# Kernel optimization log

Hardware: AMD Instinct MI355X
Metric: run time of the kernel (lower is better)

## Reference

```python
import jax, jax.numpy as jnp
import numpy as np
from jax import lax

DN = ('NCHW', 'OIHW', 'NCHW')


def convbn(x, w, s, b, relu=True):
    # conv (no bias) + folded BatchNorm affine (+ optional ReLU)
    y = lax.conv_general_dilated(x, w, (1, 1), 'SAME', dimension_numbers=DN)
    y = y * s[None, :, None, None] + b[None, :, None, None]
    return jnp.maximum(y, 0.0) if relu else y


_PARAM_SHAPES = [
    ('t', (128, 256, 3, 3)), ('l', (128, 256, 3, 3)),
    ('b', (128, 256, 3, 3)), ('r', (128, 256, 3, 3)),
    ('tl3', (256, 128, 3, 3)), ('br3', (256, 128, 3, 3)),
    ('tl1', (256, 256, 1, 1)), ('br1', (256, 256, 1, 1)),
    ('tlo', (256, 256, 3, 3)), ('bro', (256, 256, 3, 3)),
]


def setup_inputs() -> dict:
    key = jax.random.key(0)
    B, C, H, W = 8, 256, 128, 128
    ks = jax.random.split(key, 3 * len(_PARAM_SHAPES) + 1)
    inp = {'x': jax.random.normal(ks[0], (B, C, H, W), jnp.float32)}
    i = 1
    for name, shape in _PARAM_SHAPES:
        cout = shape[0]
        inp['w_' + name] = jax.random.normal(ks[i], shape, jnp.float32) * 0.05
        inp['s_' + name] = 1.0 + 0.1 * jax.random.normal(ks[i + 1], (cout,), jnp.float32)
        inp['b_' + name] = 0.1 * jax.random.normal(ks[i + 2], (cout,), jnp.float32)
        i += 3
    return inp


def reference(x, w_t, s_t, b_t, w_l, s_l, b_l, w_b, s_b, b_b, w_r, s_r, b_r,
              w_tl3, s_tl3, b_tl3, w_br3, s_br3, b_br3,
              w_tl1, s_tl1, b_tl1, w_br1, s_br1, b_br1,
              w_tlo, s_tlo, b_tlo, w_bro, s_bro, b_bro):
    # directional corner pools = (reverse-)cummax along H (axis 2) or W (axis 3)
    t = convbn(x, w_t, s_t, b_t)
    tp = lax.cummax(t, axis=2, reverse=True)   # top_pool: max over rows >= h
    l = convbn(x, w_l, s_l, b_l)
    lp = lax.cummax(l, axis=3, reverse=True)   # left_pool: max over cols >= w
    bo = convbn(x, w_b, s_b, b_b)
    bp = lax.cummax(bo, axis=2)                # bottom_pool: max over rows <= h
    r = convbn(x, w_r, s_r, b_r)
    rp = lax.cummax(r, axis=3)                 # right_pool: max over cols <= w

    tl = convbn(tp + lp, w_tl3, s_tl3, b_tl3, relu=False)
    tl = jnp.maximum(tl + convbn(x, w_tl1, s_tl1, b_tl1, relu=False), 0.0)
    out_tl = convbn(tl, w_tlo, s_tlo, b_tlo)

    br = convbn(bp + rp, w_br3, s_br3, b_br3, relu=False)
    br = jnp.maximum(br + convbn(x, w_br1, s_br1, b_br1, relu=False), 0.0)
    out_br = convbn(br, w_bro, s_bro, b_bro)
    return out_tl, out_br
```

## Files before the change

### kernel.cpp

```cpp
#include <hip/hip_runtime.h>
#include <cstdint>
#include <cstddef>


typedef float  f32x4 __attribute__((ext_vector_type(4)));
typedef float  f4v   __attribute__((ext_vector_type(4)));
typedef short  s16x8 __attribute__((ext_vector_type(8)));
typedef unsigned short u16x4 __attribute__((ext_vector_type(4)));

__device__ __forceinline__ float bf2f(unsigned short u) {
    unsigned x = ((unsigned)u) << 16;
    return __builtin_bit_cast(float, x);
}
__device__ __forceinline__ unsigned short f2bf(float f) {
    unsigned u = __builtin_bit_cast(unsigned, f);
    unsigned r = (u + 0x7fffu + ((u >> 16) & 1u)) >> 16;
    return (unsigned short)r;
}

#define GL_LDS(gp, lp) __builtin_amdgcn_global_load_lds( \
    (const __attribute__((address_space(1))) unsigned int*)(const void*)(gp), \
    (__attribute__((address_space(3))) unsigned int*)(void*)(lp), 16, 0, 0)

template<int CIN, int COUT, bool RELU, bool OUTF32, bool SWZ>
__global__ __launch_bounds__(256, 4)
void conv3_mfma(const unsigned short* __restrict__ in,
                const unsigned short* __restrict__ wpk,
                const float* __restrict__ sc, const float* __restrict__ bi,
                void* __restrict__ outv)
{
    __shared__ unsigned short lds[2][8704];
    const int tid  = threadIdx.x;
    const int lane = tid & 63;
    const int wv   = tid >> 6;
    const int c    = lane & 15;
    const int g    = lane >> 4;

    constexpr int GX  = (COUT / 128) * 2;
    int gx, hy, n;
    if (SWZ) {
        constexpr int NWG = GX * 64 * 8;
        constexpr int Q   = NWG / 8;
        const int braw = blockIdx.x + GX * (blockIdx.y + 64 * blockIdx.z);
        const int wl   = (braw & 7) * Q + (braw >> 3);
        gx = wl % GX;
        const int rest = wl / GX;
        hy = rest & 63;
        n  = rest >> 6;
    } else {
        gx = blockIdx.x; hy = blockIdx.y; n = blockIdx.z;
    }
    const int wtile  = gx & 1;
    const int octile = gx >> 1;
    const int h0   = hy * 2;
    const int w0   = wtile * 64;
    const int r    = wv >> 1;
    const int ocbase = octile * 128 + (wv & 1) * 64;
    const int ocf0   = octile * 8 + (wv & 1) * 4;

    int addrB[3];
    #pragma unroll
    for (int kx = 0; kx < 3; ++kx) {
        int ps0 = c + kx;
        addrB[kx] = r * 4224 + ps0 * 64 + ((g ^ ((ps0 >> 1) & 3)) << 4);
    }

    int so[5];
    #pragma unroll
    for (int it = 0; it < 5; ++it) {
        int u   = it * 256 + tid;
        int row = u / 264;
        int rem = u - row * 264;
        int ps  = rem >> 2;
        int s   = rem & 3;
        int icq = s ^ ((ps >> 1) & 3);
        so[it] = ((n * 130 + h0 + row) * 130 + (w0 + ps)) * CIN + icq * 8;
    }

    auto STAGE = [&](int chunk, int bsel) {
        const unsigned short* bp = in + chunk * 32;
        char* lb = (char*)lds + bsel * 17408 + tid * 16;
        #pragma unroll
        for (int it = 0; it < 4; ++it)
            GL_LDS(bp + so[it], lb + it * 4096);
        if (wv == 0)
            GL_LDS(bp + so[4], lb + 16384);
    };

    f32x4 acc[4][4];
    #pragma unroll
    for (int m = 0; m < 4; ++m)
        #pragma unroll
        for (int p = 0; p < 4; ++p) acc[m][p] = 0.0f;

    const int NC = CIN / 32;
    STAGE(0, 0);
    __syncthreads();

    for (int chunk = 0; chunk < NC; ++chunk) {
        const int cur = chunk & 1;
        if (chunk + 1 < NC) STAGE(chunk + 1, cur ^ 1);
        const char* lb = (const char*)lds + cur * 17408;
        #pragma unroll
        for (int kk = 0; kk < 9; ++kk) {
            const int ky = kk / 3, kx = kk % 3;
            s16x8 af[4], bf[4];
            #pragma unroll
            for (int m = 0; m < 4; ++m)
                af[m] = *(const s16x8*)(wpk
                    + ((size_t)((chunk * 9 + kk) * (COUT / 16) + ocf0 + m)) * 512 + lane * 8);
            #pragma unroll
            for (int p = 0; p < 4; ++p)
                bf[p] = *(const s16x8*)(lb + addrB[kx] + ky * 4224 + p * 1024);
            #pragma unroll
            for (int m = 0; m < 4; ++m)
                #pragma unroll
                for (int p = 0; p < 4; ++p)
                    acc[m][p] = __builtin_amdgcn_mfma_f32_16x16x32_bf16(af[m], bf[p], acc[m][p], 0, 0, 0);
        }
        __syncthreads();
    }

    #pragma unroll
    for (int m = 0; m < 4; ++m) {
        const int oc4 = ocbase + m * 16 + g * 4;
        const f4v s4 = *(const f4v*)(sc + oc4);
        const f4v b4 = *(const f4v*)(bi + oc4);
        #pragma unroll
        for (int p = 0; p < 4; ++p) {
            const int w = w0 + p * 16 + c;
            float y[4];
            #pragma unroll
            for (int j = 0; j < 4; ++j) {
                y[j] = acc[m][p][j] * s4[j] + b4[j];
                if (RELU) y[j] = fmaxf(y[j], 0.0f);
            }
            if (OUTF32) {
                float* op = (float*)outv + (((size_t)n * COUT + oc4) << 14) + ((h0 + r) << 7) + w;
                op[0] = y[0]; op[16384] = y[1]; op[32768] = y[2]; op[49152] = y[3];
            } else {
                u16x4 pk;
                #pragma unroll
                for (int j = 0; j < 4; ++j) pk[j] = f2bf(y[j]);
                *(u16x4*)((unsigned short*)outv
                    + ((size_t)(n * 130 + h0 + r + 1) * 130 + w + 1) * COUT + oc4) = pk;
            }
        }
    }
}

__global__ __launch_bounds__(256, 2)
void conv1_mfma(const unsigned short* __restrict__ xb,
                const unsigned short* __restrict__ w1pk,
                const float* __restrict__ sc, const float* __restrict__ bi,
                unsigned short* __restrict__ io)
{
    const int tid  = threadIdx.x;
    const int h    = blockIdx.y;
    const int n    = blockIdx.z;
    const int lane = tid & 63;
    const int wv   = tid >> 6;
    const int c    = lane & 15;
    const int g    = lane >> 4;
    const int pixbase = (wv >> 1) * 64;
    const int ocbase  = blockIdx.x * 128 + (wv & 1) * 64;
    const int ocf0    = blockIdx.x * 8 + (wv & 1) * 4;
    const size_t pixrow = ((size_t)(n * 130 + h + 1) * 130 + (pixbase + c + 1)) * 256;

    f32x4 acc[4][4];
    #pragma unroll
    for (int m = 0; m < 4; ++m)
        #pragma unroll
        for (int p = 0; p < 4; ++p) acc[m][p] = 0.0f;

    s16x8 a0[4], b0[4], a1[4], b1[4];

#define LOADC(ck, A, B) do {                                                        \
    _Pragma("unroll") for (int p = 0; p < 4; ++p)                                   \
        B[p] = *(const s16x8*)(xb + pixrow + (size_t)(16 * p) * 256 + (ck) * 32 + g * 8); \
    _Pragma("unroll") for (int m = 0; m < 4; ++m)                                   \
        A[m] = *(const s16x8*)(w1pk + ((size_t)((ck) * 16 + ocf0 + m)) * 512 + lane * 8); \
} while (0)
#define MM(A, B)                                                                    \
    _Pragma("unroll") for (int m = 0; m < 4; ++m)                                   \
        _Pragma("unroll") for (int p = 0; p < 4; ++p)                               \
            acc[m][p] = __builtin_amdgcn_mfma_f32_16x16x32_bf16(A[m], B[p], acc[m][p], 0, 0, 0)

    LOADC(0, a0, b0);
    #pragma unroll
    for (int ck = 0; ck < 8; ++ck) {
        if ((ck & 1) == 0) { if (ck < 7) LOADC(ck + 1, a1, b1); MM(a0, b0); }
        else               { if (ck < 7) LOADC(ck + 1, a0, b0); MM(a1, b1); }
    }
#undef LOADC
#undef MM

    #pragma unroll
    for (int m = 0; m < 4; ++m) {
        const int oc4 = ocbase + m * 16 + g * 4;
        const f4v s4 = *(const f4v*)(sc + oc4);
        const f4v b4 = *(const f4v*)(bi + oc4);
        #pragma unroll
        for (int p = 0; p < 4; ++p) {
            const int pix = pixbase + p * 16 + c;
            size_t idx = ((size_t)(n * 130 + h + 1) * 130 + pix + 1) * 256 + oc4;
            u16x4 old = *(const u16x4*)(io + idx);
            u16x4 pk;
            #pragma unroll
            for (int j = 0; j < 4; ++j) {
                float y = acc[m][p][j] * s4[j] + b4[j] + bf2f(old[j]);
                pk[j] = f2bf(fmaxf(y, 0.0f));
            }
            *(u16x4*)(io + idx) = pk;
        }
    }
}

__global__ __launch_bounds__(128)
void pool_h2_k(unsigned short* __restrict__ ta, unsigned short* __restrict__ tb)
{
    const int sel = blockIdx.x & 1;
    const int col = blockIdx.x >> 1;
    unsigned short* p = sel ? tb : ta;
    const int n = col >> 7, w = col & 127, cth = threadIdx.x;
    unsigned short* base = p + (((size_t)n * 130 + 1) * 130 + (w + 1)) * 128 + cth;
    const int stride = 130 * 128;
    float m = -3.402823466e+38f;
    if (sel == 0) {
        for (int gq = 0; gq < 16; ++gq) {
            const int h0 = 127 - gq * 8;
            float v[8];
            #pragma unroll
            for (int j = 0; j < 8; ++j) v[j] = bf2f(base[(size_t)(h0 - j) * stride]);
            unsigned short o[8];
            #pragma unroll
            for (int j = 0; j < 8; ++j) { m = fmaxf(m, v[j]); o[j] = f2bf(m); }
            #pragma unroll
            for (int j = 0; j < 8; ++j) base[(size_t)(h0 - j) * stride] = o[j];
        }
    } else {
        for (int gq = 0; gq < 16; ++gq) {
            const int h0 = gq * 8;
            float v[8];
            #pragma unroll
            for (int j = 0; j < 8; ++j) v[j] = bf2f(base[(size_t)(h0 + j) * stride]);
            unsigned short o[8];
            #pragma unroll
            for (int j = 0; j < 8; ++j) { m = fmaxf(m, v[j]); o[j] = f2bf(m); }
            #pragma unroll
            for (int j = 0; j < 8; ++j) base[(size_t)(h0 + j) * stride] = o[j];
        }
    }
}

__global__ __launch_bounds__(128)
void pool_w_add2_k(const unsigned short* __restrict__ la, unsigned short* __restrict__ ta,
                   const unsigned short* __restrict__ lb, unsigned short* __restrict__ tb)
{
    const int sel = blockIdx.x & 1;
    const int row = blockIdx.x >> 1;
    const unsigned short* ls = sel ? lb : la;
    unsigned short* td = sel ? tb : ta;
    const int n = row >> 7, hh = row & 127, cth = threadIdx.x;
    const size_t rowbase = ((size_t)(n * 130 + hh + 1) * 130) * 128 + cth;
    float m = -3.402823466e+38f;
    if (sel == 0) {
        for (int gq = 0; gq < 16; ++gq) {
            const int w0 = 127 - gq * 8;
            float lv[8], tv[8];
            #pragma unroll
            for (int j = 0; j < 8; ++j) {
                size_t off = rowbase + (size_t)(w0 - j + 1) * 128;
                lv[j] = bf2f(ls[off]); tv[j] = bf2f(td[off]);
            }
            unsigned short o[8];
            #pragma unroll
            for (int j = 0; j < 8; ++j) { m = fmaxf(m, lv[j]); o[j] = f2bf(m + tv[j]); }
            #pragma unroll
            for (int j = 0; j < 8; ++j) td[rowbase + (size_t)(w0 - j + 1) * 128] = o[j];
        }
    } else {
        for (int gq = 0; gq < 16; ++gq) {
            const int w0 = gq * 8;
            float lv[8], tv[8];
            #pragma unroll
            for (int j = 0; j < 8; ++j) {
                size_t off = rowbase + (size_t)(w0 + j + 1) * 128;
                lv[j] = bf2f(ls[off]); tv[j] = bf2f(td[off]);
            }
            unsigned short o[8];
            #pragma unroll
            for (int j = 0; j < 8; ++j) { m = fmaxf(m, lv[j]); o[j] = f2bf(m + tv[j]); }
            #pragma unroll
            for (int j = 0; j < 8; ++j) td[rowbase + (size_t)(w0 + j + 1) * 128] = o[j];
        }
    }
}

__global__ __launch_bounds__(256)
void padzero_k(unsigned short* __restrict__ t, int C)
{
    int idx = blockIdx.x * 256 + threadIdx.x;
    int n = blockIdx.y;
    int cpu = C >> 3;
    if (idx >= 516 * cpu) return;
    int cell = idx / cpu, cq = idx - cell * cpu;
    int h, w;
    if (cell < 260) { h = (cell < 130) ? -1 : 128; w = (cell % 130) - 1; }
    else { int j = cell - 260; w = (j < 128) ? -1 : 128; h = j & 127; }
    size_t off = (((size_t)n * 130 + h + 1) * 130 + (w + 1)) * C + cq * 8;
    uint4 z; z.x = 0; z.y = 0; z.z = 0; z.w = 0;
    *(uint4*)(t + off) = z;
}

__global__ __launch_bounds__(256)
void transform_x_k(const float* __restrict__ x, unsigned short* __restrict__ xb)
{
    __shared__ float sm[64][132];
    const int h = blockIdx.x, n = blockIdx.y, t = threadIdx.x;
    for (int cc0 = 0; cc0 < 256; cc0 += 64) {
        __syncthreads();
        {
            int ci = t >> 7, wi = t & 127;
            #pragma unroll 8
            for (int k = 0; k < 32; ++k)
                sm[ci + 2 * k][wi] = x[((size_t)(n * 256 + cc0 + ci + 2 * k) << 14) + (h << 7) + wi];
        }
        __syncthreads();
        {
            int wi = t >> 1, cq = t & 1;
            unsigned short tmp[32];
            #pragma unroll
            for (int m2 = 0; m2 < 32; ++m2) tmp[m2] = f2bf(sm[cq * 32 + m2][wi]);
            unsigned short* dst = xb + (((size_t)n * 130 + h + 1) * 130 + wi + 1) * 256 + cc0 + cq * 32;
            #pragma unroll
            for (int q = 0; q < 4; ++q) *(uint4*)(dst + q * 8) = *(const uint4*)(tmp + q * 8);
        }
    }
}

__global__ __launch_bounds__(256)
void prepack3_k(const float* __restrict__ w, unsigned short* __restrict__ dst,
                int CIN, int COUT)
{
    int idx = blockIdx.x * 256 + threadIdx.x;
    if (idx >= COUT * CIN * 9) return;
    int kk = idx % 9; int rest = idx / 9;
    int ic = rest % CIN; int oc = rest / CIN;
    float v = w[(size_t)(oc * CIN + ic) * 9 + kk];
    int chunk = ic >> 5, icr = ic & 31, gg = icr >> 3, j = icr & 7;
    int m = oc >> 4, ocr = oc & 15, ln = gg * 16 + ocr;
    size_t off = ((size_t)((chunk * 9 + kk) * (COUT / 16) + m)) * 512 + ln * 8 + j;
    dst[off] = f2bf(v);
}

__global__ __launch_bounds__(256)
void prepack1_k(const float* __restrict__ w, unsigned short* __restrict__ dst)
{
    int idx = blockIdx.x * 256 + threadIdx.x;
    if (idx >= 65536) return;
    int ic = idx & 255, oc = idx >> 8;
    float v = w[oc * 256 + ic];
    int chunk = ic >> 5, icr = ic & 31, gg = icr >> 3, j = icr & 7;
    int m = oc >> 4, ocr = oc & 15, ln = gg * 16 + ocr;
    size_t off = ((size_t)(chunk * 16 + m)) * 512 + ln * 8 + j;
    dst[off] = f2bf(v);
}

extern "C" void kernel_launch(void* const* d_in, const int* in_sizes, int n_in,
                              void* d_out, int out_size, void* d_ws, size_t ws_size,
                              hipStream_t stream)
{
    const float* x     = (const float*)d_in[0];
    const float* w_t   = (const float*)d_in[1];
    const float* s_t   = (const float*)d_in[2];
    const float* b_t   = (const float*)d_in[3];
    const float* w_l   = (const float*)d_in[4];
    const float* s_l   = (const float*)d_in[5];
    const float* b_l   = (const float*)d_in[6];
    const float* w_b   = (const float*)d_in[7];
    const float* s_b   = (const float*)d_in[8];
    const float* b_b   = (const float*)d_in[9];
    const float* w_r   = (const float*)d_in[10];
    const float* s_r   = (const float*)d_in[11];
    const float* b_r   = (const float*)d_in[12];
    const float* w_tl3 = (const float*)d_in[13];
    const float* s_tl3 = (const float*)d_in[14];
    const float* b_tl3 = (const float*)d_in[15];
    const float* w_br3 = (const float*)d_in[16];
    const float* s_br3 = (const float*)d_in[17];
    const float* b_br3 = (const float*)d_in[18];
    const float* w_tl1 = (const float*)d_in[19];
    const float* s_tl1 = (const float*)d_in[20];
    const float* b_tl1 = (const float*)d_in[21];
    const float* w_br1 = (const float*)d_in[22];
    const float* s_br1 = (const float*)d_in[23];
    const float* b_br1 = (const float*)d_in[24];
    const float* w_tlo = (const float*)d_in[25];
    const float* s_tlo = (const float*)d_in[26];
    const float* b_tlo = (const float*)d_in[27];
    const float* w_bro = (const float*)d_in[28];
    const float* s_bro = (const float*)d_in[29];
    const float* b_bro = (const float*)d_in[30];

    typedef unsigned short ush;
    const size_t T256 = (size_t)8 * 130 * 130 * 256;
    const size_t T128 = (size_t)8 * 130 * 130 * 128;

    ush* xb = (ush*)d_ws;
    ush* tt = xb + T256;
    ush* bb = tt + T128;
    ush* ll = bb + T128;
    ush* rr = ll + T128;
    ush* wq = rr + T128;
    ush* wp_t   = wq;
    ush* wp_l   = wp_t   + 294912;
    ush* wp_b   = wp_l   + 294912;
    ush* wp_r   = wp_b   + 294912;
    ush* wp_tl3 = wp_r   + 294912;
    ush* wp_br3 = wp_tl3 + 294912;
    ush* wp_tlo = wp_br3 + 294912;
    ush* wp_bro = wp_tlo + 589824;
    ush* wp_tl1 = wp_bro + 589824;
    ush* wp_br1 = wp_tl1 + 65536;
    ush* tl = ll;

    prepack3_k<<<dim3((294912 + 255) / 256), dim3(256), 0, stream>>>(w_t,   wp_t,   256, 128);
    prepack3_k<<<dim3((294912 + 255) / 256), dim3(256), 0, stream>>>(w_l,   wp_l,   256, 128);
    prepack3_k<<<dim3((294912 + 255) / 256), dim3(256), 0, stream>>>(w_b,   wp_b,   256, 128);
    prepack3_k<<<dim3((294912 + 255) / 256), dim3(256), 0, stream>>>(w_r,   wp_r,   256, 128);
    prepack3_k<<<dim3((294912 + 255) / 256), dim3(256), 0, stream>>>(w_tl3, wp_tl3, 128, 256);
    prepack3_k<<<dim3((294912 + 255) / 256), dim3(256), 0, stream>>>(w_br3, wp_br3, 128, 256);
    prepack3_k<<<dim3((589824 + 255) / 256), dim3(256), 0, stream>>>(w_tlo, wp_tlo, 256, 256);
    prepack3_k<<<dim3((589824 + 255) / 256), dim3(256), 0, stream>>>(w_bro, wp_bro, 256, 256);
    prepack1_k<<<dim3(256), dim3(256), 0, stream>>>(w_tl1, wp_tl1);
    prepack1_k<<<dim3(256), dim3(256), 0, stream>>>(w_br1, wp_br1);

    padzero_k<<<dim3(66, 8), dim3(256), 0, stream>>>(xb, 256);
    padzero_k<<<dim3(33, 8), dim3(256), 0, stream>>>(tt, 128);
    padzero_k<<<dim3(33, 8), dim3(256), 0, stream>>>(bb, 128);
    padzero_k<<<dim3(33, 8), dim3(256), 0, stream>>>(ll, 128);
    padzero_k<<<dim3(33, 8), dim3(256), 0, stream>>>(rr, 128);

    transform_x_k<<<dim3(128, 8), dim3(256), 0, stream>>>(x, xb);

    conv3_mfma<256, 128, true, false, true ><<<dim3(2, 64, 8), dim3(256), 0, stream>>>(xb, wp_t, s_t, b_t, tt);
    conv3_mfma<256, 128, true, false, true ><<<dim3(2, 64, 8), dim3(256), 0, stream>>>(xb, wp_l, s_l, b_l, ll);
    conv3_mfma<256, 128, true, false, false><<<dim3(2, 64, 8), dim3(256), 0, stream>>>(xb, wp_b, s_b, b_b, bb);
    conv3_mfma<256, 128, true, false, false><<<dim3(2, 64, 8), dim3(256), 0, stream>>>(xb, wp_r, s_r, b_r, rr);

    pool_h2_k<<<dim3(2048), dim3(128), 0, stream>>>(tt, bb);
    pool_w_add2_k<<<dim3(2048), dim3(128), 0, stream>>>(ll, tt, rr, bb);

    padzero_k<<<dim3(66, 8), dim3(256), 0, stream>>>(tl, 256);
    conv3_mfma<128, 256, false, false, true ><<<dim3(4, 64, 8), dim3(256), 0, stream>>>(tt, wp_tl3, s_tl3, b_tl3, tl);
    conv1_mfma<<<dim3(2, 128, 8), dim3(256), 0, stream>>>(xb, wp_tl1, s_tl1, b_tl1, tl);
    conv3_mfma<256, 256, true, true, true ><<<dim3(4, 64, 8), dim3(256), 0, stream>>>(tl, wp_tlo, s_tlo, b_tlo, d_out);

    conv3_mfma<128, 256, false, false, false><<<dim3(4, 64, 8), dim3(256), 0, stream>>>(bb, wp_br3, s_br3, b_br3, tl);
    conv1_mfma<<<dim3(2, 128, 8), dim3(256), 0, stream>>>(xb, wp_br1, s_br1, b_br1, tl);
    conv3_mfma<256, 256, true, true, false><<<dim3(4, 64, 8), dim3(256), 0, stream>>>(tl, wp_bro, s_bro, b_bro,
                                                                                      (float*)d_out + 33554432);
}
```

Before: 1.002 ms.

## Merge four branch convs into one interleaved launch and batch prep kernels

Replaces the four separate 256->128 conv launches with a single conv3_tlbr kernel. Its block index interleaves the four weight sets (q) so blocks reading the same input tile run close together, which should improve L2 reuse of the input activations. It also folds the ten weight-prepack launches into one kernel that additionally concatenates the branch scales and biases, and merges the five padding-zero launches into one. The new conv uses launch bounds of 4 and a fixed swizzled LDS layout; it changes the SWZ choice for the bottom/right path and the later convs, which is a correctness risk if the pooling kernels expect the old layout.

```diff
diff --git a/kernel.cpp b/kernel.cpp
--- a/kernel.cpp
+++ b/kernel.cpp
@@ -149,6 +149,118 @@
     }
 }
 
+__global__ __launch_bounds__(256, 4)
+void conv3_tlbr(const unsigned short* __restrict__ in,
+                const unsigned short* __restrict__ wq0,
+                const float* __restrict__ sA, const float* __restrict__ bA,
+                unsigned short* __restrict__ tt0)
+{
+    __shared__ unsigned short lds[2][8704];
+    const int tid  = threadIdx.x;
+    const int lane = tid & 63;
+    const int wv   = tid >> 6;
+    const int c    = lane & 15;
+    const int g    = lane >> 4;
+
+    const int b  = blockIdx.x;
+    const int x  = b & 7;
+    const int t  = b >> 3;
+    const int q  = t & 3;
+    const int ts = x + 8 * (t >> 2);
+    const int wtile = ts & 1;
+    const int hy    = (ts >> 1) & 63;
+    const int n     = ts >> 7;
+    const int h0 = hy * 2;
+    const int w0 = wtile * 64;
+    const int r  = wv >> 1;
+    const int ocbase = (wv & 1) * 64;
+    const int ocf0   = (wv & 1) * 4;
+
+    const unsigned short* wpk = wq0 + q * 294912;
+    const int outoff = ((q & 1) << 1) | (q >> 1);
+    unsigned short* outv = tt0 + (size_t)outoff * ((size_t)8 * 130 * 130 * 128);
+    const float* sc = sA + q * 128;
+    const float* bi = bA + q * 128;
+
+    int addrB[3];
+    #pragma unroll
+    for (int kx = 0; kx < 3; ++kx) {
+        int ps0 = c + kx;
+        addrB[kx] = r * 4224 + ps0 * 64 + ((g ^ ((ps0 >> 1) & 3)) << 4);
+    }
+
+    int so[5];
+    #pragma unroll
+    for (int it = 0; it < 5; ++it) {
+        int u   = it * 256 + tid;
+        int row = u / 264;
+        int rem = u - row * 264;
+        int ps  = rem >> 2;
+        int s   = rem & 3;
+        int icq = s ^ ((ps >> 1) & 3);
+        so[it] = ((n * 130 + h0 + row) * 130 + (w0 + ps)) * 256 + icq * 8;
+    }
+
+    auto STAGE = [&](int chunk, int bsel) {
+        const unsigned short* bp = in + chunk * 32;
+        char* lb = (char*)lds + bsel * 17408 + tid * 16;
+        #pragma unroll
+        for (int it = 0; it < 4; ++it)
+            GL_LDS(bp + so[it], lb + it * 4096);
+        if (wv == 0)
+            GL_LDS(bp + so[4], lb + 16384);
+    };
+
+    f32x4 acc[4][4];
+    #pragma unroll
+    for (int m = 0; m < 4; ++m)
+        #pragma unroll
+        for (int p = 0; p < 4; ++p) acc[m][p] = 0.0f;
+
+    STAGE(0, 0);
+    __syncthreads();
+
+    for (int chunk = 0; chunk < 8; ++chunk) {
+        const int cur = chunk & 1;
+        if (chunk + 1 < 8) STAGE(chunk + 1, cur ^ 1);
+        const char* lb = (const char*)lds + cur * 17408;
+        #pragma unroll
+        for (int kk = 0; kk < 9; ++kk) {
+            const int ky = kk / 3, kx = kk % 3;
+            s16x8 af[4], bf[4];
+            #pragma unroll
+            for (int m = 0; m < 4; ++m)
+                af[m] = *(const s16x8*)(wpk
+                    + ((size_t)((chunk * 9 + kk) * 8 + ocf0 + m)) * 512 + lane * 8);
+            #pragma unroll
+            for (int p = 0; p < 4; ++p)
+                bf[p] = *(const s16x8*)(lb + addrB[kx] + ky * 4224 + p * 1024);
+            #pragma unroll
+            for (int m = 0; m < 4; ++m)
+                #pragma unroll
+                for (int p = 0; p < 4; ++p)
+                    acc[m][p] = __builtin_amdgcn_mfma_f32_16x16x32_bf16(af[m], bf[p], acc[m][p], 0, 0, 0);
+        }
+        __syncthreads();
+    }
+
+    #pragma unroll
+    for (int m = 0; m < 4; ++m) {
+        const int oc4 = ocbase + m * 16 + g * 4;
+        const f4v s4 = *(const f4v*)(sc + oc4);
+        const f4v b4 = *(const f4v*)(bi + oc4);
+        #pragma unroll
+        for (int p = 0; p < 4; ++p) {
+            const int w = w0 + p * 16 + c;
+            u16x4 pk;
+            #pragma unroll
+            for (int j = 0; j < 4; ++j)
+                pk[j] = f2bf(fmaxf(acc[m][p][j] * s4[j] + b4[j], 0.0f));
+            *(u16x4*)(outv + ((size_t)(n * 130 + h0 + r + 1) * 130 + w + 1) * 128 + oc4) = pk;
+        }
+    }
+}
+
 __global__ __launch_bounds__(256, 2)
 void conv1_mfma(const unsigned short* __restrict__ xb,
                 const unsigned short* __restrict__ w1pk,
@@ -314,6 +426,26 @@
 }
 
 __global__ __launch_bounds__(256)
+void padzero_all_k(unsigned short* xb, unsigned short* tt, unsigned short* bb,
+                   unsigned short* ll, unsigned short* rr)
+{
+    const int id = blockIdx.y;
+    unsigned short* t = id == 0 ? xb : (id == 1 ? tt : (id == 2 ? bb : (id == 3 ? ll : rr)));
+    const int C = id == 0 ? 256 : 128;
+    int idx = blockIdx.x * 256 + threadIdx.x;
+    int n = blockIdx.z;
+    int cpu = C >> 3;
+    if (idx >= 516 * cpu) return;
+    int cell = idx / cpu, cq = idx - cell * cpu;
+    int h, w;
+    if (cell < 260) { h = (cell < 130) ? -1 : 128; w = (cell % 130) - 1; }
+    else { int j = cell - 260; w = (j < 128) ? -1 : 128; h = j & 127; }
+    size_t off = (((size_t)n * 130 + h + 1) * 130 + (w + 1)) * C + cq * 8;
+    uint4 z; z.x = 0; z.y = 0; z.z = 0; z.w = 0;
+    *(uint4*)(t + off) = z;
+}
+
+__global__ __launch_bounds__(256)
 void transform_x_k(const float* __restrict__ x, unsigned short* __restrict__ xb)
 {
     __shared__ float sm[64][132];
@@ -339,32 +471,44 @@
     }
 }
 
+struct PrepArgs {
+    const float* w[10];
+    unsigned short* dst[10];
+    const float* sv[4];
+    const float* bv[4];
+    float* sA; float* bA;
+};
+
 __global__ __launch_bounds__(256)
-void prepack3_k(const float* __restrict__ w, unsigned short* __restrict__ dst,
-                int CIN, int COUT)
-{
+void prepack_all_k(PrepArgs a)
+{
+    const int id = blockIdx.y;
     int idx = blockIdx.x * 256 + threadIdx.x;
+    if (id == 10) {
+        if (idx < 512) {
+            a.sA[idx] = a.sv[idx >> 7][idx & 127];
+            a.bA[idx] = a.bv[idx >> 7][idx & 127];
+        }
+        return;
+    }
+    if (id >= 8) {
+        if (idx >= 65536) return;
+        int ic = idx & 255, oc = idx >> 8;
+        float v = a.w[id][oc * 256 + ic];
+        int chunk = ic >> 5, icr = ic & 31, gg = icr >> 3, j = icr & 7;
+        int m = oc >> 4, ocr = oc & 15, ln = gg * 16 + ocr;
+        a.dst[id][((size_t)(chunk * 16 + m)) * 512 + ln * 8 + j] = f2bf(v);
+        return;
+    }
+    const int CIN  = (id < 4) ? 256 : ((id < 6) ? 128 : 256);
+    const int COUT = (id < 4) ? 128 : 256;
     if (idx >= COUT * CIN * 9) return;
     int kk = idx % 9; int rest = idx / 9;
     int ic = rest % CIN; int oc = rest / CIN;
-    float v = w[(size_t)(oc * CIN + ic) * 9 + kk];
+    float v = a.w[id][(size_t)(oc * CIN + ic) * 9 + kk];
     int chunk = ic >> 5, icr = ic & 31, gg = icr >> 3, j = icr & 7;
     int m = oc >> 4, ocr = oc & 15, ln = gg * 16 + ocr;
-    size_t off = ((size_t)((chunk * 9 + kk) * (COUT / 16) + m)) * 512 + ln * 8 + j;
-    dst[off] = f2bf(v);
-}
-
-__global__ __launch_bounds__(256)
-void prepack1_k(const float* __restrict__ w, unsigned short* __restrict__ dst)
-{
-    int idx = blockIdx.x * 256 + threadIdx.x;
-    if (idx >= 65536) return;
-    int ic = idx & 255, oc = idx >> 8;
-    float v = w[oc * 256 + ic];
-    int chunk = ic >> 5, icr = ic & 31, gg = icr >> 3, j = icr & 7;
-    int m = oc >> 4, ocr = oc & 15, ln = gg * 16 + ocr;
-    size_t off = ((size_t)(chunk * 16 + m)) * 512 + ln * 8 + j;
-    dst[off] = f2bf(v);
+    a.dst[id][((size_t)((chunk * 9 + kk) * (COUT / 16) + m)) * 512 + ln * 8 + j] = f2bf(v);
 }
 
 extern "C" void kernel_launch(void* const* d_in, const int* in_sizes, int n_in,
@@ -423,42 +567,36 @@
     ush* wp_bro = wp_tlo + 589824;
     ush* wp_tl1 = wp_bro + 589824;
     ush* wp_br1 = wp_tl1 + 65536;
+    float* sA   = (float*)(wp_br1 + 65536);
+    float* bA   = sA + 512;
     ush* tl = ll;
 
-    prepack3_k<<<dim3((294912 + 255) / 256), dim3(256), 0, stream>>>(w_t,   wp_t,   256, 128);
-    prepack3_k<<<dim3((294912 + 255) / 256), dim3(256), 0, stream>>>(w_l,   wp_l,   256, 128);
-    prepack3_k<<<dim3((294912 + 255) / 256), dim3(256), 0, stream>>>(w_b,   wp_b,   256, 128);
-    prepack3_k<<<dim3((294912 + 255) / 256), dim3(256), 0, stream>>>(w_r,   wp_r,   256, 128);
-    prepack3_k<<<dim3((294912 + 255) / 256), dim3(256), 0, stream>>>(w_tl3, wp_tl3, 128, 256);
-    prepack3_k<<<dim3((294912 + 255) / 256), dim3(256), 0, stream>>>(w_br3, wp_br3, 128, 256);
-    prepack3_k<<<dim3((589824 + 255) / 256), dim3(256), 0, stream>>>(w_tlo, wp_tlo, 256, 256);
-    prepack3_k<<<dim3((589824 + 255) / 256), dim3(256), 0, stream>>>(w_bro, wp_bro, 256, 256);
-    prepack1_k<<<dim3(256), dim3(256), 0, stream>>>(w_tl1, wp_tl1);
-    prepack1_k<<<dim3(256), dim3(256), 0, stream>>>(w_br1, wp_br1);
-
-    padzero_k<<<dim3(66, 8), dim3(256), 0, stream>>>(xb, 256);
-    padzero_k<<<dim3(33, 8), dim3(256), 0, stream>>>(tt, 128);
-    padzero_k<<<dim3(33, 8), dim3(256), 0, stream>>>(bb, 128);
-    padzero_k<<<dim3(33, 8), dim3(256), 0, stream>>>(ll, 128);
-    padzero_k<<<dim3(33, 8), dim3(256), 0, stream>>>(rr, 128);
-
+    PrepArgs pa;
+    pa.w[0] = w_t;  pa.w[1] = w_l;  pa.w[2] = w_b;  pa.w[3] = w_r;
+    pa.w[4] = w_tl3; pa.w[5] = w_br3; pa.w[6] = w_tlo; pa.w[7] = w_bro;
+    pa.w[8] = w_tl1; pa.w[9] = w_br1;
+    pa.dst[0] = wp_t;  pa.dst[1] = wp_l;  pa.dst[2] = wp_b;  pa.dst[3] = wp_r;
+    pa.dst[4] = wp_tl3; pa.dst[5] = wp_br3; pa.dst[6] = wp_tlo; pa.dst[7] = wp_bro;
+    pa.dst[8] = wp_tl1; pa.dst[9] = wp_br1;
+    pa.sv[0] = s_t; pa.sv[1] = s_l; pa.sv[2] = s_b; pa.sv[3] = s_r;
+    pa.bv[0] = b_t; pa.bv[1] = b_l; pa.bv[2] = b_b; pa.bv[3] = b_r;
+    pa.sA = sA; pa.bA = bA;
+    prepack_all_k<<<dim3(2304, 11), dim3(256), 0, stream>>>(pa);
+    padzero_all_k<<<dim3(516, 5, 8), dim3(256), 0, stream>>>(xb, tt, bb, ll, rr);
     transform_x_k<<<dim3(128, 8), dim3(256), 0, stream>>>(x, xb);
 
-    conv3_mfma<256, 128, true, false, true ><<<dim3(2, 64, 8), dim3(256), 0, stream>>>(xb, wp_t, s_t, b_t, tt);
-    conv3_mfma<256, 128, true, false, true ><<<dim3(2, 64, 8), dim3(256), 0, stream>>>(xb, wp_l, s_l, b_l, ll);
-    conv3_mfma<256, 128, true, false, false><<<dim3(2, 64, 8), dim3(256), 0, stream>>>(xb, wp_b, s_b, b_b, bb);
-    conv3_mfma<256, 128, true, false, false><<<dim3(2, 64, 8), dim3(256), 0, stream>>>(xb, wp_r, s_r, b_r, rr);
+    conv3_tlbr<<<dim3(4096), dim3(256), 0, stream>>>(xb, wp_t, sA, bA, tt);
 
     pool_h2_k<<<dim3(2048), dim3(128), 0, stream>>>(tt, bb);
     pool_w_add2_k<<<dim3(2048), dim3(128), 0, stream>>>(ll, tt, rr, bb);
 
     padzero_k<<<dim3(66, 8), dim3(256), 0, stream>>>(tl, 256);
-    conv3_mfma<128, 256, false, false, true ><<<dim3(4, 64, 8), dim3(256), 0, stream>>>(tt, wp_tl3, s_tl3, b_tl3, tl);
+    conv3_mfma<128, 256, false, false, true><<<dim3(4, 64, 8), dim3(256), 0, stream>>>(tt, wp_tl3, s_tl3, b_tl3, tl);
     conv1_mfma<<<dim3(2, 128, 8), dim3(256), 0, stream>>>(xb, wp_tl1, s_tl1, b_tl1, tl);
-    conv3_mfma<256, 256, true, true, true ><<<dim3(4, 64, 8), dim3(256), 0, stream>>>(tl, wp_tlo, s_tlo, b_tlo, d_out);
-
-    conv3_mfma<128, 256, false, false, false><<<dim3(4, 64, 8), dim3(256), 0, stream>>>(bb, wp_br3, s_br3, b_br3, tl);
+    conv3_mfma<256, 256, true, true, true><<<dim3(4, 64, 8), dim3(256), 0, stream>>>(tl, wp_tlo, s_tlo, b_tlo, d_out);
+
+    conv3_mfma<128, 256, false, false, true><<<dim3(4, 64, 8), dim3(256), 0, stream>>>(bb, wp_br3, s_br3, b_br3, tl);
     conv1_mfma<<<dim3(2, 128, 8), dim3(256), 0, stream>>>(xb, wp_br1, s_br1, b_br1, tl);
-    conv3_mfma<256, 256, true, true, false><<<dim3(4, 64, 8), dim3(256), 0, stream>>>(tl, wp_bro, s_bro, b_bro,
-                                                                                      (float*)d_out + 33554432);
-}
+    conv3_mfma<256, 256, true, true, true><<<dim3(4, 64, 8), dim3(256), 0, stream>>>(tl, wp_bro, s_bro, b_bro,
+                                                                                     (float*)d_out + 33554432);
+}
```

New measurement: 924.8 us. 1.08x faster.
